# Kernel tuning notes

Hardware: AMD Instinct MI355X
Metric: run time of the kernel (lower is better)

## Reference

```python
import jax, jax.numpy as jnp
import numpy as np

B_IMG = 2
N_PROP = 2000
N_GT = 16
C_FEAT = 256
H_FEAT = 128
W_FEAT = 128
IMG = 1024.0
NUM_CLASSES = 2
BG_THRESH = 0.5          # fg==bg==0.5 -> BETWEEN_THRESHOLDS band is empty
BPI = 512                # batch_size_per_image
NUM_POS_MAX = int(BPI * 0.25)
ENC_W = (1.0, 1.0, 1.0, 1.0, 1.0)
SCALE = 1.0 / 8.0        # feature stride
POOL = 7
SR = 2                   # sampling_ratio
BETA = 1.0 / 9.0
HID = 1024


def _make_boxes(key, shape_prefix, img=IMG):
    kc, ks = jax.random.split(key)
    c = jax.random.uniform(kc, shape_prefix + (2,), minval=0.0, maxval=img)
    s = jax.random.uniform(ks, shape_prefix + (2,), minval=20.0, maxval=200.0)
    lo = jnp.clip(c - 0.5 * s, 0.0, img - 2.0)
    hi = jnp.clip(c + 0.5 * s, lo + 1.0, img)
    return jnp.concatenate([lo, hi], axis=-1)  # [.., x1,y1,x2,y2]


def setup_inputs():
    key = jax.random.key(0)
    ks = jax.random.split(key, 12)
    features = jax.random.normal(ks[0], (B_IMG, C_FEAT, H_FEAT, W_FEAT), dtype=jnp.float32)
    proposals = _make_boxes(ks[1], (B_IMG, N_PROP))
    gt_boxes = _make_boxes(ks[2], (B_IMG, N_GT))
    gt_labels = jax.random.randint(ks[3], (B_IMG, N_GT), 1, NUM_CLASSES, dtype=jnp.int32)
    ka, kb, kt = jax.random.split(ks[4], 3)
    a = jax.random.uniform(ka, (B_IMG, N_GT), minval=10.0, maxval=60.0)
    b = jax.random.uniform(kb, (B_IMG, N_GT), minval=5.0, maxval=30.0)
    th = jax.random.uniform(kt, (B_IMG, N_GT), minval=-np.pi / 2, maxval=np.pi / 2)
    exy = 0.5 * (gt_boxes[..., :2] + gt_boxes[..., 2:])
    gt_ellipses = jnp.stack([a, b, exy[..., 0], exy[..., 1], th], axis=-1)
    d_in = C_FEAT * POOL * POOL
    w1 = jax.random.normal(ks[5], (d_in, HID), dtype=jnp.float32) * 0.02
    b1 = jnp.zeros((HID,), jnp.float32)
    w2 = jax.random.normal(ks[6], (HID, HID), dtype=jnp.float32) * 0.02
    b2 = jnp.zeros((HID,), jnp.float32)
    wc = jax.random.normal(ks[7], (HID, NUM_CLASSES), dtype=jnp.float32) * 0.02
    bc = jnp.zeros((NUM_CLASSES,), jnp.float32)
    wr = jax.random.normal(ks[8], (HID, NUM_CLASSES * 6), dtype=jnp.float32) * 0.02
    br = jnp.zeros((NUM_CLASSES * 6,), jnp.float32)
    return dict(features=features, proposals=proposals, gt_boxes=gt_boxes,
                gt_labels=gt_labels, gt_ellipses=gt_ellipses,
                w1=w1, b1=b1, w2=w2, b2=b2, wc=wc, bc=bc, wr=wr, br=br)


def box_iou(b1, b2):  # [G,4], [P,4] -> [G,P]
    a1 = (b1[:, 2] - b1[:, 0]) * (b1[:, 3] - b1[:, 1])
    a2 = (b2[:, 2] - b2[:, 0]) * (b2[:, 3] - b2[:, 1])
    lt = jnp.maximum(b1[:, None, :2], b2[None, :, :2])
    rb = jnp.minimum(b1[:, None, 2:], b2[None, :, 2:])
    wh = jnp.clip(rb - lt, 0.0)
    inter = wh[..., 0] * wh[..., 1]
    return inter / (a1[:, None] + a2[None, :] - inter)


def encode_ellipses(ell, boxes):  # ell [..,5]=(a,b,cx,cy,theta), boxes [..,4] -> [..,6]
    a, b, ex, ey, th = (ell[..., i] for i in range(5))
    w = jnp.maximum(boxes[..., 2] - boxes[..., 0], 1.0)
    h = jnp.maximum(boxes[..., 3] - boxes[..., 1], 1.0)
    cx = 0.5 * (boxes[..., 0] + boxes[..., 2])
    cy = 0.5 * (boxes[..., 1] + boxes[..., 3])
    wx, wy, wa, wb, wt = ENC_W
    dx = wx * (ex - cx) / w
    dy = wy * (ey - cy) / h
    da = wa * jnp.log(jnp.maximum(2.0 * a, 1e-3) / w)
    db = wb * jnp.log(jnp.maximum(2.0 * b, 1e-3) / h)
    return jnp.stack([dx, dy, da, db, wt * jnp.sin(2.0 * th), wt * jnp.cos(2.0 * th)], axis=-1)


def roi_align(fmap, rois):  # [C,H,W], [R,4] -> [R,C,POOL,POOL]
    C, H, W = fmap.shape
    r = rois * SCALE
    x1, y1, x2, y2 = r[:, 0], r[:, 1], r[:, 2], r[:, 3]
    bw = jnp.maximum(x2 - x1, 1.0) / POOL
    bh = jnp.maximum(y2 - y1, 1.0) / POOL
    S = POOL * SR
    off = (jnp.arange(S, dtype=jnp.float32) + 0.5) / SR  # bin-unit sample offsets
    ys = jnp.clip(y1[:, None] + off[None, :] * bh[:, None], 0.0, H - 1.0)  # [R,S]
    xs = jnp.clip(x1[:, None] + off[None, :] * bw[:, None], 0.0, W - 1.0)
    y0 = jnp.clip(jnp.floor(ys), 0, H - 2).astype(jnp.int32)
    x0 = jnp.clip(jnp.floor(xs), 0, W - 2).astype(jnp.int32)
    ly = ys - y0
    lx = xs - x0
    Ya, Yb = y0[:, :, None], (y0 + 1)[:, :, None]  # [R,S,1]
    Xa, Xb = x0[:, None, :], (x0 + 1)[:, None, :]  # [R,1,S]
    v00 = fmap[:, Ya, Xa]; v01 = fmap[:, Ya, Xb]   # [C,R,S,S]
    v10 = fmap[:, Yb, Xa]; v11 = fmap[:, Yb, Xb]
    wy1 = ly[:, :, None]; wy0 = 1.0 - wy1
    wx1 = lx[:, None, :]; wx0 = 1.0 - wx1
    val = v00 * (wy0 * wx0) + v01 * (wy0 * wx1) + v10 * (wy1 * wx0) + v11 * (wy1 * wx1)
    R = rois.shape[0]
    pooled = val.reshape(C, R, POOL, SR, POOL, SR).mean(axis=(3, 5))
    return pooled.transpose(1, 0, 2, 3)


def reference(features, proposals, gt_boxes, gt_labels, gt_ellipses,
              w1, b1, w2, b2, wc, bc, wr, br):
    B = features.shape[0]
    # add_gt_proposals
    props = jnp.concatenate([proposals, gt_boxes], axis=1)            # [B,P,4]
    # assign_targets_to_proposals: IoU + Matcher (fg=bg=0.5)
    iou = jax.vmap(box_iou)(gt_boxes, props)                          # [B,G,P]
    matched_vals = iou.max(axis=1)
    matches = iou.argmax(axis=1)                                      # [B,P]
    lab = jnp.take_along_axis(gt_labels, matches, axis=1)
    lab = jnp.where(matched_vals < BG_THRESH, 0, lab)                 # background
    # BalancedPositiveNegativeSampler (deterministic, fixed-shape):
    # cap positives at NUM_POS_MAX by random rank, fill rest with random negatives
    rand = jax.random.uniform(jax.random.key(42), lab.shape)
    is_pos = lab > 0
    is_neg = lab == 0
    pos_s = jnp.where(is_pos, rand, -1e9)
    rank = jnp.argsort(jnp.argsort(-pos_s, axis=1), axis=1)
    capped = is_pos & (rank < NUM_POS_MAX)
    prio = jnp.where(capped, rand + 2.0, jnp.where(is_neg, rand, -1e9))
    _, idx = jax.lax.top_k(prio, BPI)                                 # [B,512]
    boxes = jnp.take_along_axis(props, idx[..., None], axis=1)        # [B,512,4]
    labels = jnp.take_along_axis(lab, idx, axis=1)                    # [B,512]
    m = jnp.take_along_axis(matches, idx, axis=1)
    ell = jnp.take_along_axis(gt_ellipses, m[..., None], axis=1)      # [B,512,5]
    targets = encode_ellipses(ell, boxes)                             # [B,512,6]
    # RoIAlign + TwoMLPHead + predictor
    pooled = jax.vmap(roi_align)(features, boxes)                     # [B,512,C,7,7]
    N = B * BPI
    x = pooled.reshape(N, -1)
    x = jax.nn.relu(x @ w1 + b1)
    x = jax.nn.relu(x @ w2 + b2)
    logits = x @ wc + bc                                              # [N,2]
    reg = (x @ wr + br).reshape(N, NUM_CLASSES, 6)
    # ellipse_rcnn_loss
    labels_f = labels.reshape(N)
    t = targets.reshape(N, 6)
    ce = -jnp.take_along_axis(jax.nn.log_softmax(logits, axis=-1), labels_f[:, None], axis=1).mean()
    pred = jnp.take_along_axis(reg, labels_f[:, None, None], axis=1)[:, 0]  # [N,6]
    d = jnp.abs(pred - t)
    sl1 = jnp.where(d < BETA, 0.5 * d * d / BETA, d - 0.5 * BETA)
    reg_loss = jnp.sum(sl1 * (labels_f > 0)[:, None].astype(sl1.dtype)) / N
    return jnp.stack([ce, reg_loss])
```

## Files before the change

### kernel.cpp

```cpp
#include <hip/hip_runtime.h>
#include <hip/hip_bf16.h>
#include <math.h>

#define B_IMG   2
#define N_PROP  2000
#define N_GT    16
#define NPROPS  2016
#define C_FEAT  256
#define H_FEAT  128
#define W_FEAT  128
#define HWF     (H_FEAT*W_FEAT)
#define POOL    7
#define BPI     512
#define NPOSMAX 128
#define NSEL    (B_IMG*BPI)
#define K1      (C_FEAT*POOL*POOL)
#define K1P     12800
#define HID     1024
#define NHEAD   14
#define SPLITK1 8

typedef short bf16x8f __attribute__((ext_vector_type(8)));
typedef float f32x4f  __attribute__((ext_vector_type(4)));
typedef short short4v __attribute__((ext_vector_type(4)));

__device__ __forceinline__ void threefry2x32(unsigned k0, unsigned k1,
                                             unsigned& x0, unsigned& x1) {
  unsigned ks[3] = {k0, k1, k0 ^ k1 ^ 0x1BD11BDAu};
  const int R0[4] = {13, 15, 26, 6};
  const int R1[4] = {17, 29, 16, 24};
  x0 += ks[0]; x1 += ks[1];
#pragma unroll
  for (int g = 0; g < 5; g++) {
    const int* rot = (g & 1) ? R1 : R0;
#pragma unroll
    for (int r = 0; r < 4; r++) {
      x0 += x1;
      x1 = (x1 << rot[r]) | (x1 >> (32 - rot[r]));
      x1 ^= x0;
    }
    x0 += ks[(g + 1) % 3];
    x1 += ks[(g + 2) % 3] + (unsigned)(g + 1);
  }
}

#define PRE_SAMPLE   2
#define PRE_TRANS    (PRE_SAMPLE + 2048)
#define PRE_CAST1    (PRE_TRANS + 3136)
#define PRE_CAST0    (PRE_CAST1 + 256)
#define PRE_TOTAL    (PRE_CAST0 + 512)

__global__ __launch_bounds__(256) void k_pre(const float* __restrict__ proposals,
                                             const float* __restrict__ gt_boxes,
                                             const int* __restrict__ gt_labels,
                                             const float* __restrict__ features,
                                             const float* __restrict__ w1,
                                             const float* __restrict__ w2,
                                             float* __restrict__ prio,
                                             int* __restrict__ plab,
                                             int* __restrict__ matches,
                                             __hip_bfloat16* __restrict__ featT,
                                             __hip_bfloat16* __restrict__ W1T,
                                             __hip_bfloat16* __restrict__ W2T,
                                             __hip_bfloat16* __restrict__ Xb) {
  __shared__ __align__(16) char smem[20800];
  int bid = blockIdx.x;
  int tid = threadIdx.x;
  if (bid < PRE_SAMPLE) {
    float* rs    = (float*)smem;
    float* pos_r = (float*)(smem + 8064);
    short* pos_i = (short*)(smem + 16128);
    float* gtb   = (float*)(smem + 20160);
    int*   gtl   = (int*)(smem + 20416);
    int*   cnt   = (int*)(smem + 20480);
    int b = bid;
    int base = b * NPROPS;
    if (tid == 0) *cnt = 0;
    if (tid < N_GT * 4) gtb[tid] = gt_boxes[b * N_GT * 4 + tid];
    if (tid < N_GT) gtl[tid] = gt_labels[b * N_GT + tid];
    __syncthreads();
    for (int i = tid; i < NPROPS; i += 256) {
      unsigned x0 = 0u, x1 = (unsigned)(base + i);
      threefry2x32(0u, 42u, x0, x1);
      unsigned bits = x0 ^ x1;
      float r = __uint_as_float((bits >> 9) | 0x3F800000u) - 1.0f;
      rs[i] = r;
      float p0, p1, p2, p3;
      if (i < N_PROP) {
        const float4 v = *(const float4*)(proposals + ((size_t)b * N_PROP + i) * 4);
        p0 = v.x; p1 = v.y; p2 = v.z; p3 = v.w;
      } else {
        const float* g = &gtb[(i - N_PROP) * 4];
        p0 = g[0]; p1 = g[1]; p2 = g[2]; p3 = g[3];
      }
      float a2 = (p2 - p0) * (p3 - p1);
      float best = -1.0f; int bg = 0;
#pragma unroll
      for (int g = 0; g < N_GT; g++) {
        float g0 = gtb[g*4], g1 = gtb[g*4+1], g2 = gtb[g*4+2], g3 = gtb[g*4+3];
        float a1 = (g2 - g0) * (g3 - g1);
        float wx = fmaxf(fminf(g2, p2) - fmaxf(g0, p0), 0.0f);
        float wy = fmaxf(fminf(g3, p3) - fmaxf(g1, p1), 0.0f);
        float inter = wx * wy;
        float iou = inter / (a1 + a2 - inter);
        if (iou > best) { best = iou; bg = g; }
      }
      matches[base + i] = bg;
      int lab = (best < 0.5f) ? 0 : gtl[bg];
      plab[base + i] = lab;
      if (lab > 0) {
        int s = atomicAdd(cnt, 1);
        pos_i[s] = (short)i; pos_r[s] = r;
      }
    }
    __syncthreads();
    int P = *cnt;
    for (int s = tid; s < P; s += 256) {
      int i = pos_i[s]; float ri = pos_r[s];
      int ch = 0;
      for (int j = 0; j < P; j++) {
        float rj = pos_r[j]; int ij = pos_i[j];
        ch += (rj > ri || (rj == ri && ij < i)) ? 1 : 0;
      }
      rs[i] = (ch < NPOSMAX) ? (ri + 2.0f) : -1000000000.0f;
    }
    __syncthreads();
    for (int i = tid; i < NPROPS; i += 256) prio[base + i] = rs[i];
  } else if (bid < PRE_TRANS) {
    float (*tile)[65] = (float(*)[65])smem;
    int t = bid - PRE_SAMPLE;
    int b = t >> 10;
    int rem = t & 1023;
    int c0 = (rem >> 8) * 64;
    int s0 = (rem & 255) * 64;
    const float* src = features + (size_t)b * C_FEAT * HWF;
    __hip_bfloat16* dst = featT + (size_t)b * HWF * C_FEAT;
    int hw4 = (tid & 15) * 4, cr = tid >> 4;
#pragma unroll
    for (int p = 0; p < 4; p++) {
      int c = cr + p * 16;
      float4 v = *(const float4*)(src + (size_t)(c0 + c) * HWF + s0 + hw4);
      tile[hw4 + 0][c] = v.x; tile[hw4 + 1][c] = v.y;
      tile[hw4 + 2][c] = v.z; tile[hw4 + 3][c] = v.w;
    }
    __syncthreads();
    int c4 = (tid & 15) * 4, hr = tid >> 4;
#pragma unroll
    for (int p = 0; p < 4; p++) {
      int hw = hr + p * 16;
      __hip_bfloat16 o[4] = {__float2bfloat16(tile[hw][c4]), __float2bfloat16(tile[hw][c4+1]),
                             __float2bfloat16(tile[hw][c4+2]), __float2bfloat16(tile[hw][c4+3])};
      *(short4v*)(dst + (size_t)(s0 + hw) * C_FEAT + c0 + c4) = *(short4v*)o;
    }
  } else if (bid < PRE_CAST1) {
    float (*tile)[65] = (float(*)[65])smem;
    int t = bid - PRE_TRANS;
    int p = t >> 6;
    int rem = t & 63;
    int c0 = (rem & 3) * 64;
    int n0 = (rem >> 2) * 64;
    int n4 = (tid & 15) * 4, ig = tid >> 4;
#pragma unroll
    for (int i = ig; i < 64; i += 16) {
      float4 v = *(const float4*)(w1 + (size_t)((c0 + i) * 49 + p) * HID + n0 + n4);
      tile[i][n4] = v.x; tile[i][n4 + 1] = v.y;
      tile[i][n4 + 2] = v.z; tile[i][n4 + 3] = v.w;
    }
    __syncthreads();
    int c4 = (tid & 15) * 4;
#pragma unroll
    for (int i = ig; i < 64; i += 16) {
      __hip_bfloat16 o[4] = {__float2bfloat16(tile[c4][i]), __float2bfloat16(tile[c4 + 1][i]),
                             __float2bfloat16(tile[c4 + 2][i]), __float2bfloat16(tile[c4 + 3][i])};
      *(short4v*)(W1T + (size_t)(n0 + i) * K1P + p * 256 + c0 + c4) = *(short4v*)o;
    }
  } else if (bid < PRE_CAST0) {
    float (*tile)[65] = (float(*)[65])smem;
    int t = bid - PRE_CAST1;
    int c0 = (t & 15) * 64;
    int n0 = (t >> 4) * 64;
    int n4 = (tid & 15) * 4, ig = tid >> 4;
#pragma unroll
    for (int i = ig; i < 64; i += 16) {
      float4 v = *(const float4*)(w2 + (size_t)(c0 + i) * HID + n0 + n4);
      tile[i][n4] = v.x; tile[i][n4 + 1] = v.y;
      tile[i][n4 + 2] = v.z; tile[i][n4 + 3] = v.w;
    }
    __syncthreads();
    int c4 = (tid & 15) * 4;
#pragma unroll
    for (int i = ig; i < 64; i += 16) {
      __hip_bfloat16 o[4] = {__float2bfloat16(tile[c4][i]), __float2bfloat16(tile[c4 + 1][i]),
                             __float2bfloat16(tile[c4 + 2][i]), __float2bfloat16(tile[c4 + 3][i])};
      *(short4v*)(W2T + (size_t)(n0 + i) * HID + c0 + c4) = *(short4v*)o;
    }
  } else {
    int t = bid - PRE_CAST0;
    __hip_bfloat16* buf = (t >> 8) ? W1T : Xb;
    int tt = (t & 255) * 256 + tid;
    int row = tt >> 6;
    int col4 = (tt & 63) << 2;
    short4v z = {0, 0, 0, 0};
    *(short4v*)(buf + (size_t)row * K1P + K1 + col4) = z;
  }
}

__global__ __launch_bounds__(256) void k_select(const float* __restrict__ prio,
    const float* __restrict__ proposals, const float* __restrict__ gt_boxes,
    const int* __restrict__ matches, const int* __restrict__ plab,
    const float* __restrict__ gt_ell,
    float* __restrict__ sel_boxes, int* __restrict__ sel_labels,
    float* __restrict__ targets) {
  int tid = threadIdx.x;
  int wave = tid >> 6, lane = tid & 63;
  int b = blockIdx.y;
  int base = b * NPROPS;
  int i = blockIdx.x * 4 + wave;
  float pi = prio[base + i];
  int rank = 0;
  for (int j = lane; j < NPROPS; j += 64) {
    float pj = prio[base + j];
    rank += (pj > pi || (pj == pi && j < i)) ? 1 : 0;
  }
#pragma unroll
  for (int off = 32; off > 0; off >>= 1) rank += __shfl_down(rank, off);
  if (lane != 0 || rank >= BPI) return;
  int slot = b * BPI + rank;
  float p0, p1, p2, p3;
  if (i < N_PROP) {
    const float* p = proposals + ((size_t)b * N_PROP + i) * 4;
    p0 = p[0]; p1 = p[1]; p2 = p[2]; p3 = p[3];
  } else {
    const float* p = gt_boxes + ((size_t)b * N_GT + (i - N_PROP)) * 4;
    p0 = p[0]; p1 = p[1]; p2 = p[2]; p3 = p[3];
  }
  sel_boxes[slot * 4 + 0] = p0;
  sel_boxes[slot * 4 + 1] = p1;
  sel_boxes[slot * 4 + 2] = p2;
  sel_boxes[slot * 4 + 3] = p3;
  int lb = plab[base + i];
  sel_labels[slot] = lb;
  int m = matches[base + i];
  const float* e = gt_ell + ((size_t)b * N_GT + m) * 5;
  float ea = e[0], eb = e[1], ex = e[2], ey = e[3], eth = e[4];
  float w = fmaxf(p2 - p0, 1.0f), h = fmaxf(p3 - p1, 1.0f);
  float cx = 0.5f * (p0 + p2), cy = 0.5f * (p1 + p3);
  float* t = targets + (size_t)slot * 6;
  t[0] = (ex - cx) / w;
  t[1] = (ey - cy) / h;
  t[2] = logf(fmaxf(2.0f * ea, 0.001f) / w);
  t[3] = logf(fmaxf(2.0f * eb, 0.001f) / h);
  t[4] = sinf(2.0f * eth);
  t[5] = cosf(2.0f * eth);
}

__global__ __launch_bounds__(256) void k_roialign(const __hip_bfloat16* __restrict__ featT,
                                                  const float* __restrict__ sel_boxes,
                                                  __hip_bfloat16* __restrict__ X) {
  int n = blockIdx.x;
  int py = blockIdx.y;
  int t = threadIdx.x;
  int px = t >> 5;
  int lane32 = t & 31;
  int c = lane32 << 3;
  int b = n >> 9;
  const float* bx = sel_boxes + (size_t)n * 4;
  float x1 = bx[0] * 0.125f, y1 = bx[1] * 0.125f;
  float x2 = bx[2] * 0.125f, y2 = bx[3] * 0.125f;
  float bw = fmaxf(x2 - x1, 1.0f) / 7.0f;
  float bh = fmaxf(y2 - y1, 1.0f) / 7.0f;
  if (px >= 7) return;
  const __hip_bfloat16* base = featT + (size_t)b * HWF * C_FEAT;
  int y0A[2]; float lyA[2];
#pragma unroll
  for (int sy = 0; sy < 2; sy++) {
    float off = ((float)(py * 2 + sy) + 0.5f) * 0.5f;
    float ys = fminf(fmaxf(y1 + off * bh, 0.0f), 127.0f);
    int y0 = (int)fminf(fmaxf(floorf(ys), 0.0f), 126.0f);
    y0A[sy] = y0; lyA[sy] = ys - (float)y0;
  }
  float acc[8] = {};
#pragma unroll
  for (int sx = 0; sx < 2; sx++) {
    float off = ((float)(px * 2 + sx) + 0.5f) * 0.5f;
    float xs = fminf(fmaxf(x1 + off * bw, 0.0f), 127.0f);
    int x0 = (int)fminf(fmaxf(floorf(xs), 0.0f), 126.0f);
    float lx = xs - (float)x0;
#pragma unroll
    for (int sy = 0; sy < 2; sy++) {
      int y0 = y0A[sy]; float ly = lyA[sy];
      const __hip_bfloat16* p = base + ((size_t)(y0 * W_FEAT + x0)) * C_FEAT + c;
      bf16x8f s00 = *(const bf16x8f*)p;
      bf16x8f s01 = *(const bf16x8f*)(p + C_FEAT);
      bf16x8f s10 = *(const bf16x8f*)(p + W_FEAT * C_FEAT);
      bf16x8f s11 = *(const bf16x8f*)(p + W_FEAT * C_FEAT + C_FEAT);
      float w00 = (1.0f - ly) * (1.0f - lx), w01 = (1.0f - ly) * lx;
      float w10 = ly * (1.0f - lx), w11 = ly * lx;
#pragma unroll
      for (int q = 0; q < 8; q++) {
        float v00 = __uint_as_float(((unsigned)(unsigned short)s00[q]) << 16);
        float v01 = __uint_as_float(((unsigned)(unsigned short)s01[q]) << 16);
        float v10 = __uint_as_float(((unsigned)(unsigned short)s10[q]) << 16);
        float v11 = __uint_as_float(((unsigned)(unsigned short)s11[q]) << 16);
        acc[q] += v00 * w00 + v01 * w01 + v10 * w10 + v11 * w11;
      }
    }
  }
  __hip_bfloat16 o[8];
#pragma unroll
  for (int q = 0; q < 8; q++) o[q] = __float2bfloat16(acc[q] * 0.25f);
  *(bf16x8f*)&X[(size_t)n * K1P + (size_t)(py * 7 + px) * C_FEAT + c] = *(bf16x8f*)o;
}

__device__ __forceinline__ void gld_lds16(const __hip_bfloat16* g, __hip_bfloat16* l) {
  __builtin_amdgcn_global_load_lds(
      (const __attribute__((address_space(1))) void*)g,
      (__attribute__((address_space(3))) void*)l, 16, 0, 0);
}

#define G1_KC   1600
#define G1_NKT  25
#define G1_ABUF 16384
#define G1_BUFE 24576

__global__ __launch_bounds__(512, 1) void k_gemm1(const __hip_bfloat16* __restrict__ A,
                                                  const __hip_bfloat16* __restrict__ BT,
                                                  __hip_bfloat16* __restrict__ Pb) {
  __shared__ __align__(16) __hip_bfloat16 lds[3 * G1_BUFE];
  const int lin = blockIdx.x;
  const int pair = (lin & 7) + ((lin >> 6) << 3);
  const int m0 = (pair & 3) * 256;
  const int kz = pair >> 2;
  const int n0 = ((lin >> 3) & 7) * 128;
  const int kbeg = kz * G1_KC;
  const int tid = threadIdx.x;
  const int wave = tid >> 6, lane = tid & 63;
  const int wm = (wave & 3) * 64, wn = (wave >> 2) * 64;
  const int lm = lane & 15, quad = lane >> 4;

  f32x4f acc[4][4] = {};

  auto stage = [&](int kt, int sb) {
    const int kcol = kbeg + kt * 64;
    __hip_bfloat16* lb = lds + sb * G1_BUFE;
#pragma unroll
    for (int u = 0; u < 4; ++u) {
      int idx = tid + u * 512;
      int r = idx >> 3, g = (idx & 7) ^ (r & 7);
      gld_lds16(A + (size_t)(m0 + r) * K1P + kcol + g * 8, lb + idx * 8);
    }
#pragma unroll
    for (int u = 0; u < 2; ++u) {
      int idx = tid + u * 512;
      int r = idx >> 3, g = (idx & 7) ^ (r & 7);
      gld_lds16(BT + (size_t)(n0 + r) * K1P + kcol + g * 8, lb + G1_ABUF + idx * 8);
    }
  };

  stage(0, 0);
  stage(1, 1);
  asm volatile("s_waitcnt vmcnt(6)" ::: "memory");
  __builtin_amdgcn_s_barrier();

  int buf = 0;
  for (int kt = 0; kt < G1_NKT; ++kt) {
    int sb = buf + 2; if (sb >= 3) sb -= 3;
    if (kt + 2 < G1_NKT) stage(kt + 2, sb);
    const __hip_bfloat16* Ab = lds + buf * G1_BUFE;
    const __hip_bfloat16* Bb = Ab + G1_ABUF;
    bf16x8f af[4][2], bf[4][2];
#pragma unroll
    for (int i = 0; i < 4; ++i)
#pragma unroll
      for (int s = 0; s < 2; ++s)
        af[i][s] = *(const bf16x8f*)(Ab + (wm + i * 16 + lm) * 64 +
                                     (((s << 2) + quad) ^ (lm & 7)) * 8);
#pragma unroll
    for (int j = 0; j < 4; ++j)
#pragma unroll
      for (int s = 0; s < 2; ++s)
        bf[j][s] = *(const bf16x8f*)(Bb + (wn + j * 16 + lm) * 64 +
                                     (((s << 2) + quad) ^ (lm & 7)) * 8);
    __builtin_amdgcn_s_setprio(1);
#pragma unroll
    for (int s = 0; s < 2; ++s)
#pragma unroll
      for (int i = 0; i < 4; ++i)
#pragma unroll
        for (int j = 0; j < 4; ++j)
          acc[i][j] = __builtin_amdgcn_mfma_f32_16x16x32_bf16(af[i][s], bf[j][s], acc[i][j], 0, 0, 0);
    __builtin_amdgcn_s_setprio(0);
    if (kt < G1_NKT - 1) {
      if (kt < G1_NKT - 2) asm volatile("s_waitcnt vmcnt(6)" ::: "memory");
      else                 asm volatile("s_waitcnt vmcnt(0)" ::: "memory");
      __builtin_amdgcn_s_barrier();
    }
    buf = (buf == 2) ? 0 : buf + 1;
  }

  int tileoff = ((m0 >> 8) * 8 + (n0 >> 7)) * 32768;
  __hip_bfloat16* dst = Pb + ((size_t)kz << 20) + tileoff + wave * 4096 + lane * 4;
#pragma unroll
  for (int i = 0; i < 4; ++i)
#pragma unroll
    for (int j = 0; j < 4; ++j) {
      __hip_bfloat16 o[4] = {__float2bfloat16(acc[i][j][0]), __float2bfloat16(acc[i][j][1]),
                             __float2bfloat16(acc[i][j][2]), __float2bfloat16(acc[i][j][3])};
      *(short4v*)(dst + (i * 4 + j) * 256) = *(short4v*)o;
    }
}

__global__ __launch_bounds__(256) void k_reduce16(const __hip_bfloat16* __restrict__ Pb,
                                                  const float* __restrict__ bias,
                                                  __hip_bfloat16* __restrict__ O) {
  int m4 = blockIdx.x >> 2;
  int n  = (blockIdx.x & 3) * 256 + threadIdx.x;
  int m0i = m4 >> 6, wavem = (m4 >> 4) & 3, i = (m4 >> 2) & 3, quad = m4 & 3;
  int n0i = n >> 7, wn = (n >> 6) & 1, j = (n >> 4) & 3, lm = n & 15;
  int wave = wavem + wn * 4;
  int elem = (m0i * 8 + n0i) * 32768 + wave * 4096 + (i * 4 + j) * 256 + (quad * 16 + lm) * 4;
  float s0 = 0.0f, s1 = 0.0f, s2 = 0.0f, s3 = 0.0f;
#pragma unroll
  for (int z = 0; z < SPLITK1; z++) {
    short4v v = *(const short4v*)(Pb + ((size_t)z << 20) + elem);
    s0 += __uint_as_float(((unsigned)(unsigned short)v[0]) << 16);
    s1 += __uint_as_float(((unsigned)(unsigned short)v[1]) << 16);
    s2 += __uint_as_float(((unsigned)(unsigned short)v[2]) << 16);
    s3 += __uint_as_float(((unsigned)(unsigned short)v[3]) << 16);
  }
  float bv = bias[n];
  int m = m4 * 4;
  O[(size_t)(m + 0) * HID + n] = __float2bfloat16(fmaxf(s0 + bv, 0.0f));
  O[(size_t)(m + 1) * HID + n] = __float2bfloat16(fmaxf(s1 + bv, 0.0f));
  O[(size_t)(m + 2) * HID + n] = __float2bfloat16(fmaxf(s2 + bv, 0.0f));
  O[(size_t)(m + 3) * HID + n] = __float2bfloat16(fmaxf(s3 + bv, 0.0f));
}

#define G2_NKT  16
#define G2_ABUF 8192
#define G2_BUFE 16384
#define H2P     129

__global__ __launch_bounds__(256, 1) void k_gemm2h(const __hip_bfloat16* __restrict__ A,
                                                   const __hip_bfloat16* __restrict__ BT,
                                                   const float* __restrict__ b2,
                                                   const float* __restrict__ wc,
                                                   const float* __restrict__ wr,
                                                   float* __restrict__ Ypart) {
  __shared__ __align__(16) char smem[3 * G2_BUFE * 2];
  __hip_bfloat16* slds = (__hip_bfloat16*)smem;
  float* h2 = (float*)smem;
  float* wh = (float*)(smem + 128 * H2P * 4);
  const int m0 = (blockIdx.x >> 3) * 128;
  const int nb = blockIdx.x & 7;
  const int n0 = nb * 128;
  const int tid = threadIdx.x;
  const int wave = tid >> 6, lane = tid & 63;
  const int wm = (wave & 1) * 64, wn = (wave >> 1) * 64;
  const int lm = lane & 15, quad = lane >> 4;

  f32x4f acc[4][4] = {};

  auto stage = [&](int kt, int sb) {
    const int kcol = kt * 64;
    __hip_bfloat16* lb = slds + sb * G2_BUFE;
#pragma unroll
    for (int u = 0; u < 4; ++u) {
      int idx = tid + u * 256;
      int r = idx >> 3, g = (idx & 7) ^ (r & 7);
      gld_lds16(A + (size_t)(m0 + r) * HID + kcol + g * 8, lb + idx * 8);
    }
#pragma unroll
    for (int u = 0; u < 4; ++u) {
      int idx = tid + u * 256;
      int r = idx >> 3, g = (idx & 7) ^ (r & 7);
      gld_lds16(BT + (size_t)(n0 + r) * HID + kcol + g * 8, lb + G2_ABUF + idx * 8);
    }
  };

  stage(0, 0);
  stage(1, 1);
  asm volatile("s_waitcnt vmcnt(8)" ::: "memory");
  __builtin_amdgcn_s_barrier();

  int buf = 0;
  for (int kt = 0; kt < G2_NKT; ++kt) {
    int sb = buf + 2; if (sb >= 3) sb -= 3;
    if (kt + 2 < G2_NKT) stage(kt + 2, sb);
    const __hip_bfloat16* Ab = slds + buf * G2_BUFE;
    const __hip_bfloat16* Bb = Ab + G2_ABUF;
    bf16x8f af[4][2], bf[4][2];
#pragma unroll
    for (int i = 0; i < 4; ++i)
#pragma unroll
      for (int s = 0; s < 2; ++s)
        af[i][s] = *(const bf16x8f*)(Ab + (wm + i * 16 + lm) * 64 +
                                     (((s << 2) + quad) ^ (lm & 7)) * 8);
#pragma unroll
    for (int j = 0; j < 4; ++j)
#pragma unroll
      for (int s = 0; s < 2; ++s)
        bf[j][s] = *(const bf16x8f*)(Bb + (wn + j * 16 + lm) * 64 +
                                     (((s << 2) + quad) ^ (lm & 7)) * 8);
    __builtin_amdgcn_s_setprio(1);
#pragma unroll
    for (int s = 0; s < 2; ++s)
#pragma unroll
      for (int i = 0; i < 4; ++i)
#pragma unroll
        for (int j = 0; j < 4; ++j)
          acc[i][j] = __builtin_amdgcn_mfma_f32_16x16x32_bf16(af[i][s], bf[j][s], acc[i][j], 0, 0, 0);
    __builtin_amdgcn_s_setprio(0);
    if (kt < G2_NKT - 1) {
      if (kt < G2_NKT - 2) asm volatile("s_waitcnt vmcnt(8)" ::: "memory");
      else                 asm volatile("s_waitcnt vmcnt(0)" ::: "memory");
      __builtin_amdgcn_s_barrier();
    }
    buf = (buf == 2) ? 0 : buf + 1;
  }
  __syncthreads();

  float bb[4];
#pragma unroll
  for (int j = 0; j < 4; ++j) bb[j] = b2[n0 + wn + j * 16 + lm];
#pragma unroll
  for (int i = 0; i < 4; ++i)
#pragma unroll
    for (int j = 0; j < 4; ++j) {
      int col = wn + j * 16 + lm;
#pragma unroll
      for (int r = 0; r < 4; ++r) {
        int row = wm + i * 16 + quad * 4 + r;
        h2[row * H2P + col] = fmaxf(acc[i][j][r] + bb[j], 0.0f);
      }
    }
  for (int idx = tid; idx < 128 * 14; idx += 256) {
    int nl = idx / 14, j = idx - nl * 14;
    wh[idx] = (j < 2) ? wc[(size_t)(n0 + nl) * 2 + j]
                      : wr[(size_t)(n0 + nl) * 12 + (j - 2)];
  }
  __syncthreads();
  int rrow = tid & 127, j0 = (tid >> 7) * 7;
  float s[7] = {};
#pragma unroll 4
  for (int k = 0; k < 128; ++k) {
    float h = h2[rrow * H2P + k];
    const float* w = wh + k * 14 + j0;
#pragma unroll
    for (int j = 0; j < 7; ++j) s[j] += h * w[j];
  }
  float* yp = Ypart + ((size_t)nb * NSEL + m0 + rrow) * 16 + j0;
#pragma unroll
  for (int j = 0; j < 7; ++j) yp[j] = s[j];
}

__global__ __launch_bounds__(1024) void k_head_loss(const float* __restrict__ Ypart,
                                                    const float* __restrict__ bc,
                                                    const float* __restrict__ br,
                                                    const int* __restrict__ sel_labels,
                                                    const float* __restrict__ T,
                                                    float* __restrict__ out) {
  __shared__ float sc[1024];
  __shared__ float sr[1024];
  int n = threadIdx.x;
  float y[14];
#pragma unroll
  for (int j = 0; j < 14; ++j) y[j] = (j < 2) ? bc[j] : br[j - 2];
#pragma unroll
  for (int nb = 0; nb < 8; ++nb) {
    const float* p = Ypart + ((size_t)nb * NSEL + n) * 16;
    float4 v0 = *(const float4*)(p + 0);
    float4 v1 = *(const float4*)(p + 4);
    float4 v2 = *(const float4*)(p + 8);
    float2 v3 = *(const float2*)(p + 12);
    y[0] += v0.x; y[1] += v0.y; y[2] += v0.z; y[3] += v0.w;
    y[4] += v1.x; y[5] += v1.y; y[6] += v1.z; y[7] += v1.w;
    y[8] += v2.x; y[9] += v2.y; y[10] += v2.z; y[11] += v2.w;
    y[12] += v3.x; y[13] += v3.y;
  }
  int lb = sel_labels[n];
  float mx = fmaxf(y[0], y[1]);
  float lse = mx + logf(expf(y[0] - mx) + expf(y[1] - mx));
  float ce = lse - (lb ? y[1] : y[0]);
  float reg = 0.0f;
  if (lb > 0) {
    const float beta = 1.0f / 9.0f;
    const float* t = T + (size_t)n * 6;
#pragma unroll
    for (int j = 0; j < 6; j++) {
      float d = fabsf(y[2 + lb * 6 + j] - t[j]);
      reg += (d < beta) ? (0.5f * d * d / beta) : (d - 0.5f * beta);
    }
  }
  sc[n] = ce; sr[n] = reg;
  __syncthreads();
  for (int sft = 512; sft > 0; sft >>= 1) {
    if (n < sft) { sc[n] += sc[n + sft]; sr[n] += sr[n + sft]; }
    __syncthreads();
  }
  if (n == 0) {
    out[0] = sc[0] * (1.0f / 1024.0f);
    out[1] = sr[0] * (1.0f / 1024.0f);
  }
}

extern "C" void kernel_launch(void* const* d_in, const int* in_sizes, int n_in,
                              void* d_out, int out_size, void* d_ws, size_t ws_size,
                              hipStream_t stream) {
  const float* features  = (const float*)d_in[0];
  const float* proposals = (const float*)d_in[1];
  const float* gt_boxes  = (const float*)d_in[2];
  const int*   gt_labels = (const int*)d_in[3];
  const float* gt_ell    = (const float*)d_in[4];
  const float* w1 = (const float*)d_in[5];
  const float* b1 = (const float*)d_in[6];
  const float* w2 = (const float*)d_in[7];
  const float* b2 = (const float*)d_in[8];
  const float* wc = (const float*)d_in[9];
  const float* bc = (const float*)d_in[10];
  const float* wr = (const float*)d_in[11];
  const float* br = (const float*)d_in[12];
  float* out = (float*)d_out;

  char* ws = (char*)d_ws;
  size_t off = 0;
  auto take = [&](size_t bytes) -> void* {
    void* p = ws + off;
    off = (off + bytes + 255) & ~(size_t)255;
    return p;
  };
  __hip_bfloat16* Pb = (__hip_bfloat16*)take((size_t)16 * (1 << 20) * 2);
  __hip_bfloat16* featT = Pb;
  __hip_bfloat16* Xb  = (__hip_bfloat16*)take((size_t)NSEL * K1P * 2);
  __hip_bfloat16* W1T = (__hip_bfloat16*)take((size_t)HID * K1P * 2);
  __hip_bfloat16* W2T = (__hip_bfloat16*)take((size_t)HID * HID * 2);
  __hip_bfloat16* H1b = (__hip_bfloat16*)take((size_t)NSEL * HID * 2);
  float* Ypart     = (float*)take((size_t)8 * NSEL * 16 * 4);
  int*   matches   = (int*)take((size_t)B_IMG * NPROPS * 4);
  int*   plab      = (int*)take((size_t)B_IMG * NPROPS * 4);
  float* prio      = (float*)take((size_t)B_IMG * NPROPS * 4);
  float* sel_boxes = (float*)take((size_t)NSEL * 4 * 4);
  int*   sel_lab   = (int*)take((size_t)NSEL * 4);
  float* targets   = (float*)take((size_t)NSEL * 6 * 4);

  k_pre<<<PRE_TOTAL, 256, 0, stream>>>(proposals, gt_boxes, gt_labels, features,
                                       w1, w2, prio, plab, matches,
                                       featT, W1T, W2T, Xb);
  k_select<<<dim3(NPROPS / 4, B_IMG), 256, 0, stream>>>(prio, proposals, gt_boxes,
                                                        matches, plab, gt_ell,
                                                        sel_boxes, sel_lab, targets);
  k_roialign<<<dim3(NSEL, POOL), 256, 0, stream>>>(featT, sel_boxes, Xb);

  k_gemm1<<<256, 512, 0, stream>>>(Xb, W1T, Pb);
  k_reduce16<<<1024, 256, 0, stream>>>(Pb, b1, H1b);
  k_gemm2h<<<64, 256, 0, stream>>>(H1b, W2T, b2, wc, wr, Ypart);
  k_head_loss<<<1, 1024, 0, stream>>>(Ypart, bc, br, sel_lab, targets, out);
}
```

Measured before the change: 243.6 us.

## Fuse head loss into gemm2 via last-block counter and widen blocks to 512

Removes the separate single-block loss kernel. A global atomic counter picks the last finishing gemm2 block, and that block reduces the partial head outputs and computes the CE and smooth-L1 loss. gemm2 blocks also grow from 256 to 512 threads, giving each wave a 64x32 tile instead of 64x64, which halves the staging loads per thread. This saves one kernel launch and raises waves per CU, at the cost of threadfence and atomic overhead. The counter is never reset and relies on modulo 64, so it stays correct only if the grid size stays at 64.

```diff
diff --git a/kernel.cpp b/kernel.cpp
--- a/kernel.cpp
+++ b/kernel.cpp
@@ -441,13 +441,20 @@
 #define G2_BUFE 16384
 #define H2P     129
 
-__global__ __launch_bounds__(256, 1) void k_gemm2h(const __hip_bfloat16* __restrict__ A,
+__global__ __launch_bounds__(512, 1) void k_gemm2h(const __hip_bfloat16* __restrict__ A,
                                                    const __hip_bfloat16* __restrict__ BT,
                                                    const float* __restrict__ b2,
                                                    const float* __restrict__ wc,
                                                    const float* __restrict__ wr,
-                                                   float* __restrict__ Ypart) {
+                                                   float* __restrict__ Ypart,
+                                                   const float* __restrict__ bc,
+                                                   const float* __restrict__ br,
+                                                   const int* __restrict__ sel_labels,
+                                                   const float* __restrict__ T,
+                                                   float* __restrict__ out,
+                                                   int* __restrict__ loss_cnt) {
   __shared__ __align__(16) char smem[3 * G2_BUFE * 2];
+  __shared__ int lastf;
   __hip_bfloat16* slds = (__hip_bfloat16*)smem;
   float* h2 = (float*)smem;
   float* wh = (float*)(smem + 128 * H2P * 4);
@@ -456,23 +463,23 @@
   const int n0 = nb * 128;
   const int tid = threadIdx.x;
   const int wave = tid >> 6, lane = tid & 63;
-  const int wm = (wave & 1) * 64, wn = (wave >> 1) * 64;
+  const int wm = (wave & 1) * 64, wn = (wave >> 1) * 32;
   const int lm = lane & 15, quad = lane >> 4;
 
-  f32x4f acc[4][4] = {};
+  f32x4f acc[4][2] = {};
 
   auto stage = [&](int kt, int sb) {
     const int kcol = kt * 64;
     __hip_bfloat16* lb = slds + sb * G2_BUFE;
 #pragma unroll
-    for (int u = 0; u < 4; ++u) {
-      int idx = tid + u * 256;
+    for (int u = 0; u < 2; ++u) {
+      int idx = tid + u * 512;
       int r = idx >> 3, g = (idx & 7) ^ (r & 7);
       gld_lds16(A + (size_t)(m0 + r) * HID + kcol + g * 8, lb + idx * 8);
     }
 #pragma unroll
-    for (int u = 0; u < 4; ++u) {
-      int idx = tid + u * 256;
+    for (int u = 0; u < 2; ++u) {
+      int idx = tid + u * 512;
       int r = idx >> 3, g = (idx & 7) ^ (r & 7);
       gld_lds16(BT + (size_t)(n0 + r) * HID + kcol + g * 8, lb + G2_ABUF + idx * 8);
     }
@@ -480,7 +487,7 @@
 
   stage(0, 0);
   stage(1, 1);
-  asm volatile("s_waitcnt vmcnt(8)" ::: "memory");
+  asm volatile("s_waitcnt vmcnt(4)" ::: "memory");
   __builtin_amdgcn_s_barrier();
 
   int buf = 0;
@@ -489,7 +496,7 @@
     if (kt + 2 < G2_NKT) stage(kt + 2, sb);
     const __hip_bfloat16* Ab = slds + buf * G2_BUFE;
     const __hip_bfloat16* Bb = Ab + G2_ABUF;
-    bf16x8f af[4][2], bf[4][2];
+    bf16x8f af[4][2], bf[2][2];
 #pragma unroll
     for (int i = 0; i < 4; ++i)
 #pragma unroll
@@ -497,7 +504,7 @@
         af[i][s] = *(const bf16x8f*)(Ab + (wm + i * 16 + lm) * 64 +
                                      (((s << 2) + quad) ^ (lm & 7)) * 8);
 #pragma unroll
-    for (int j = 0; j < 4; ++j)
+    for (int j = 0; j < 2; ++j)
 #pragma unroll
       for (int s = 0; s < 2; ++s)
         bf[j][s] = *(const bf16x8f*)(Bb + (wn + j * 16 + lm) * 64 +
@@ -508,11 +515,11 @@
 #pragma unroll
       for (int i = 0; i < 4; ++i)
 #pragma unroll
-        for (int j = 0; j < 4; ++j)
+        for (int j = 0; j < 2; ++j)
           acc[i][j] = __builtin_amdgcn_mfma_f32_16x16x32_bf16(af[i][s], bf[j][s], acc[i][j], 0, 0, 0);
     __builtin_amdgcn_s_setprio(0);
     if (kt < G2_NKT - 1) {
-      if (kt < G2_NKT - 2) asm volatile("s_waitcnt vmcnt(8)" ::: "memory");
+      if (kt < G2_NKT - 2) asm volatile("s_waitcnt vmcnt(4)" ::: "memory");
       else                 asm volatile("s_waitcnt vmcnt(0)" ::: "memory");
       __builtin_amdgcn_s_barrier();
     }
@@ -520,13 +527,13 @@
   }
   __syncthreads();
 
-  float bb[4];
-#pragma unroll
-  for (int j = 0; j < 4; ++j) bb[j] = b2[n0 + wn + j * 16 + lm];
+  float bb[2];
+#pragma unroll
+  for (int j = 0; j < 2; ++j) bb[j] = b2[n0 + wn + j * 16 + lm];
 #pragma unroll
   for (int i = 0; i < 4; ++i)
 #pragma unroll
-    for (int j = 0; j < 4; ++j) {
+    for (int j = 0; j < 2; ++j) {
       int col = wn + j * 16 + lm;
 #pragma unroll
       for (int r = 0; r < 4; ++r) {
@@ -534,71 +541,77 @@
         h2[row * H2P + col] = fmaxf(acc[i][j][r] + bb[j], 0.0f);
       }
     }
-  for (int idx = tid; idx < 128 * 14; idx += 256) {
+  for (int idx = tid; idx < 128 * 14; idx += 512) {
     int nl = idx / 14, j = idx - nl * 14;
     wh[idx] = (j < 2) ? wc[(size_t)(n0 + nl) * 2 + j]
                       : wr[(size_t)(n0 + nl) * 12 + (j - 2)];
   }
   __syncthreads();
-  int rrow = tid & 127, j0 = (tid >> 7) * 7;
-  float s[7] = {};
+  {
+    int rrow = tid & 127, jg = tid >> 7;
+    int j0 = jg * 4, jn = (jg == 3) ? 2 : 4;
+    float s[4] = {};
 #pragma unroll 4
-  for (int k = 0; k < 128; ++k) {
-    float h = h2[rrow * H2P + k];
-    const float* w = wh + k * 14 + j0;
-#pragma unroll
-    for (int j = 0; j < 7; ++j) s[j] += h * w[j];
-  }
-  float* yp = Ypart + ((size_t)nb * NSEL + m0 + rrow) * 16 + j0;
-#pragma unroll
-  for (int j = 0; j < 7; ++j) yp[j] = s[j];
-}
-
-__global__ __launch_bounds__(1024) void k_head_loss(const float* __restrict__ Ypart,
-                                                    const float* __restrict__ bc,
-                                                    const float* __restrict__ br,
-                                                    const int* __restrict__ sel_labels,
-                                                    const float* __restrict__ T,
-                                                    float* __restrict__ out) {
-  __shared__ float sc[1024];
-  __shared__ float sr[1024];
-  int n = threadIdx.x;
-  float y[14];
-#pragma unroll
-  for (int j = 0; j < 14; ++j) y[j] = (j < 2) ? bc[j] : br[j - 2];
-#pragma unroll
-  for (int nb = 0; nb < 8; ++nb) {
-    const float* p = Ypart + ((size_t)nb * NSEL + n) * 16;
-    float4 v0 = *(const float4*)(p + 0);
-    float4 v1 = *(const float4*)(p + 4);
-    float4 v2 = *(const float4*)(p + 8);
-    float2 v3 = *(const float2*)(p + 12);
-    y[0] += v0.x; y[1] += v0.y; y[2] += v0.z; y[3] += v0.w;
-    y[4] += v1.x; y[5] += v1.y; y[6] += v1.z; y[7] += v1.w;
-    y[8] += v2.x; y[9] += v2.y; y[10] += v2.z; y[11] += v2.w;
-    y[12] += v3.x; y[13] += v3.y;
-  }
-  int lb = sel_labels[n];
-  float mx = fmaxf(y[0], y[1]);
-  float lse = mx + logf(expf(y[0] - mx) + expf(y[1] - mx));
-  float ce = lse - (lb ? y[1] : y[0]);
-  float reg = 0.0f;
-  if (lb > 0) {
-    const float beta = 1.0f / 9.0f;
-    const float* t = T + (size_t)n * 6;
-#pragma unroll
-    for (int j = 0; j < 6; j++) {
-      float d = fabsf(y[2 + lb * 6 + j] - t[j]);
-      reg += (d < beta) ? (0.5f * d * d / beta) : (d - 0.5f * beta);
-    }
-  }
-  sc[n] = ce; sr[n] = reg;
+    for (int k = 0; k < 128; ++k) {
+      float h = h2[rrow * H2P + k];
+      const float* w = wh + k * 14 + j0;
+#pragma unroll
+      for (int j = 0; j < 4; ++j) s[j] += h * w[j];
+    }
+    float* yp = Ypart + ((size_t)nb * NSEL + m0 + rrow) * 16 + j0;
+    for (int j = 0; j < jn; ++j) yp[j] = s[j];
+  }
   __syncthreads();
-  for (int sft = 512; sft > 0; sft >>= 1) {
-    if (n < sft) { sc[n] += sc[n + sft]; sr[n] += sr[n + sft]; }
+  if (tid == 0) {
+    __threadfence();
+    int old = atomicAdd(loss_cnt, 1);
+    lastf = ((old & 63) == 63) ? 1 : 0;
+  }
+  __syncthreads();
+  if (!lastf) return;
+  __threadfence();
+  float* sc = (float*)smem;
+  float* sr = sc + 512;
+  float ce_s = 0.0f, rg_s = 0.0f;
+#pragma unroll
+  for (int half = 0; half < 2; ++half) {
+    int n = tid + half * 512;
+    float y[14];
+#pragma unroll
+    for (int j = 0; j < 14; ++j) y[j] = (j < 2) ? bc[j] : br[j - 2];
+#pragma unroll
+    for (int nb2 = 0; nb2 < 8; ++nb2) {
+      const float* p = Ypart + ((size_t)nb2 * NSEL + n) * 16;
+      float4 v0 = *(const float4*)(p + 0);
+      float4 v1 = *(const float4*)(p + 4);
+      float4 v2 = *(const float4*)(p + 8);
+      float2 v3 = *(const float2*)(p + 12);
+      y[0] += v0.x; y[1] += v0.y; y[2] += v0.z; y[3] += v0.w;
+      y[4] += v1.x; y[5] += v1.y; y[6] += v1.z; y[7] += v1.w;
+      y[8] += v2.x; y[9] += v2.y; y[10] += v2.z; y[11] += v2.w;
+      y[12] += v3.x; y[13] += v3.y;
+    }
+    int lb = sel_labels[n];
+    float mx = fmaxf(y[0], y[1]);
+    float lse = mx + logf(expf(y[0] - mx) + expf(y[1] - mx));
+    ce_s += lse - (lb ? y[1] : y[0]);
+    if (lb > 0) {
+      const float beta = 1.0f / 9.0f;
+      const float* t = T + (size_t)n * 6;
+#pragma unroll
+      for (int j = 0; j < 6; j++) {
+        float d = fabsf(y[2 + lb * 6 + j] - t[j]);
+        rg_s += (d < beta) ? (0.5f * d * d / beta) : (d - 0.5f * beta);
+      }
+    }
+  }
+  sc[tid] = ce_s; sr[tid] = rg_s;
+  __syncthreads();
+  for (int sft = 256; sft > 0; sft >>= 1) {
+    if (tid < sft) { sc[tid] += sc[tid + sft]; sr[tid] += sr[tid + sft]; }
     __syncthreads();
   }
-  if (n == 0) {
+  if (tid == 0) {
     out[0] = sc[0] * (1.0f / 1024.0f);
     out[1] = sr[0] * (1.0f / 1024.0f);
   }
@@ -642,6 +655,7 @@
   float* sel_boxes = (float*)take((size_t)NSEL * 4 * 4);
   int*   sel_lab   = (int*)take((size_t)NSEL * 4);
   float* targets   = (float*)take((size_t)NSEL * 6 * 4);
+  int*   loss_cnt  = (int*)take(256);
 
   k_pre<<<PRE_TOTAL, 256, 0, stream>>>(proposals, gt_boxes, gt_labels, features,
                                        w1, w2, prio, plab, matches,
@@ -653,6 +667,6 @@
 
   k_gemm1<<<256, 512, 0, stream>>>(Xb, W1T, Pb);
   k_reduce16<<<1024, 256, 0, stream>>>(Pb, b1, H1b);
-  k_gemm2h<<<64, 256, 0, stream>>>(H1b, W2T, b2, wc, wr, Ypart);
-  k_head_loss<<<1, 1024, 0, stream>>>(Ypart, bc, br, sel_lab, targets, out);
-}
+  k_gemm2h<<<64, 512, 0, stream>>>(H1b, W2T, b2, wc, wr, Ypart,
+                                   bc, br, sel_lab, targets, out, loss_cnt);
+}
```

Measured after the change: 237.3 us. -2.6%, faster.
